# Performance work log

Hardware: AMD Instinct MI355X
Metric: run time of the kernel (lower is better)

Reference implementation:

```python
import jax, jax.numpy as jnp
import numpy as np

# Module config (matches init_kwargs)
IN_F = 4096
OUT_F = 12288
R = 16
ENABLE_LORA = [True, False, True]
N_BLOCKS = len(ENABLE_LORA)          # 3 fused output blocks (Q, K, V)
GROUPS = sum(ENABLE_LORA)            # 2 LoRA-enabled blocks
OUT_PG = OUT_F // N_BLOCKS           # 4096 rows per block
ENABLED_IDX = np.array([i for i, e in enumerate(ENABLE_LORA) if e])  # [0, 2]


def setup_inputs() -> dict:
    key = jax.random.key(0)
    kx, ka, kb = jax.random.split(key, 3)
    x = jax.random.normal(kx, (2, 512, IN_F), dtype=jnp.float32)
    # kaiming_uniform-like scale is irrelevant for correctness testing; use randn
    weight_A = jax.random.normal(ka, (GROUPS * R, IN_F), dtype=jnp.float32) * 0.02
    weight_B = jax.random.normal(kb, (OUT_PG * GROUPS, R), dtype=jnp.float32) * 0.02
    return {"x": x, "weight_A": weight_A, "weight_B": weight_B}


def _merge_AB(weight_A, weight_B):
    # grouped conv1d with kernel size 1 == per-group matmul B_g @ A_g
    A = weight_A.reshape(GROUPS, R, IN_F)          # (g, r, in)
    B = weight_B.reshape(GROUPS, OUT_PG, R)        # (g, out_pg, r)
    delta = jnp.einsum('gor,gri->goi', B, A)       # (g, out_pg, in)
    # zero_pad: scatter enabled blocks into the full (N_BLOCKS, out_pg, in) weight
    W = jnp.zeros((N_BLOCKS, OUT_PG, IN_F), dtype=delta.dtype)
    W = W.at[jnp.asarray(ENABLED_IDX)].set(delta)
    return W.reshape(OUT_F, IN_F)


def reference(x, weight_A, weight_B):
    W = _merge_AB(weight_A, weight_B)              # (out_f, in_f), full materialization as in torch
    return jnp.einsum('bsi,oi->bso', x, W)         # F.linear(x, W), no bias (lora_bias=False)
```

## Files before the change

kernel.cpp:

```cpp
#include <hip/hip_runtime.h>
#include <hip/hip_bf16.h>

#define IN_F   4096
#define OUT_F  12288
#define OUT_PG 4096
#define M_ROWS 1024
#define R2     32
#define KS     16

__global__ __launch_bounds__(256) void lora_a_kernel(
    const float* __restrict__ x, const float* __restrict__ wA,
    float* __restrict__ Tpart, float* __restrict__ out) {
  constexpr int SLICE = IN_F / KS;
  constexpr int ZC    = OUT_PG / KS;
  __shared__ float As[R2 * SLICE];

  const int t = threadIdx.x;
  const int l = t & 63;
  const int w = t >> 6;
  const int ks = blockIdx.x;
  const int row0 = blockIdx.y * 16 + w * 4;
  const int kb = ks * SLICE;

  {
    const int zrow0 = blockIdx.y * 16;
    const int zcol0 = OUT_PG + ks * ZC;
    const float4 z = {0.f, 0.f, 0.f, 0.f};
#pragma unroll
    for (int i = 0; i < 4; ++i) {
      const int idx = t + i * 256;
      const int zr = idx >> 6;
      const int zc = (idx & 63) * 4;
      *reinterpret_cast<float4*>(&out[(zrow0 + zr) * OUT_F + zcol0 + zc]) = z;
    }
  }

#pragma unroll
  for (int i = 0; i < 8; ++i) {
    const int f = t * 4 + i * 1024;
    const int r = f >> 8, kk = f & 255;
    *reinterpret_cast<float4*>(&As[f]) =
        *reinterpret_cast<const float4*>(&wA[r * IN_F + kb + kk]);
  }
  __syncthreads();

  float4 xv[4];
#pragma unroll
  for (int m = 0; m < 4; ++m)
    xv[m] = *reinterpret_cast<const float4*>(&x[(row0 + m) * IN_F + kb + l * 4]);

  float acc[4][32];
#pragma unroll
  for (int m = 0; m < 4; ++m)
#pragma unroll
    for (int r = 0; r < 32; ++r) acc[m][r] = 0.f;

#pragma unroll
  for (int r = 0; r < 32; ++r) {
    const float4 av = *reinterpret_cast<const float4*>(&As[r * SLICE + l * 4]);
#pragma unroll
    for (int m = 0; m < 4; ++m)
      acc[m][r] += xv[m].x * av.x + xv[m].y * av.y + xv[m].z * av.z + xv[m].w * av.w;
  }

  float v[4];
#pragma unroll
  for (int m2 = 0; m2 < 4; ++m2) {
#pragma unroll
    for (int m = 16; m >= 1; m >>= 1) {
#pragma unroll
      for (int i = 0; i < m; ++i) {
        const float a = acc[m2][i], b = acc[m2][i + m];
        const float mine   = (l & m) ? b : a;
        const float theirs = (l & m) ? a : b;
        acc[m2][i] = mine + __shfl_xor(theirs, m, 64);
      }
    }
    v[m2] = acc[m2][0] + __shfl_xor(acc[m2][0], 32, 64);
  }
#pragma unroll
  for (int p = 0; p < 2; ++p) {
    const float outv = (l < 32) ? v[2 * p] : v[2 * p + 1];
    Tpart[(ks * M_ROWS + row0 + 2 * p + (l >> 5)) * R2 + (l & 31)] = outv;
  }
}

__global__ __launch_bounds__(256) void lora_b_kernel(
    const float* __restrict__ Tpart, const float* __restrict__ wB,
    float* __restrict__ out) {
  const int t = threadIdx.x;
  const int bx = blockIdx.x;
  const int by = blockIdx.y;
  const int g = bx >> 4;
  const int jbase = (bx & 15) << 8;
  const int colbase = g ? (2 * OUT_PG + jbase) : jbase;
  const int rbase = by << 5;
  const int cq = t & 63;
  const int rowg = t >> 6;

  __shared__ float BsT[16 * 260];
  __shared__ float Ts[32 * 16];

#pragma unroll
  for (int i = 0; i < 4; ++i) {
    const int idx = t + i * 256;
    const int c = idx >> 2, r0 = (idx & 3) * 4;
    const float4 v = *reinterpret_cast<const float4*>(
        &wB[(g * OUT_PG + jbase + c) * 16 + r0]);
    BsT[(r0 + 0) * 260 + c] = v.x;
    BsT[(r0 + 1) * 260 + c] = v.y;
    BsT[(r0 + 2) * 260 + c] = v.z;
    BsT[(r0 + 3) * 260 + c] = v.w;
  }
  if (t < 128) {
    const int row = t >> 2, q = t & 3;
    float4 s0 = {0.f, 0.f, 0.f, 0.f}, s1 = {0.f, 0.f, 0.f, 0.f};
#pragma unroll
    for (int ks = 0; ks < KS; ks += 2) {
      const float4 v0 = *reinterpret_cast<const float4*>(
          &Tpart[((ks + 0) * M_ROWS + rbase + row) * R2 + g * 16 + q * 4]);
      const float4 v1 = *reinterpret_cast<const float4*>(
          &Tpart[((ks + 1) * M_ROWS + rbase + row) * R2 + g * 16 + q * 4]);
      s0.x += v0.x; s0.y += v0.y; s0.z += v0.z; s0.w += v0.w;
      s1.x += v1.x; s1.y += v1.y; s1.z += v1.z; s1.w += v1.w;
    }
    const float4 s = {s0.x + s1.x, s0.y + s1.y, s0.z + s1.z, s0.w + s1.w};
    *reinterpret_cast<float4*>(&Ts[row * 16 + q * 4]) = s;
  }
  __syncthreads();

  float4 brow[16];
#pragma unroll
  for (int r = 0; r < 16; ++r)
    brow[r] = *reinterpret_cast<const float4*>(&BsT[r * 260 + cq * 4]);

#pragma unroll
  for (int rr = 0; rr < 8; ++rr) {
    const int rowl = rowg * 8 + rr;
    float ts[16];
#pragma unroll
    for (int q = 0; q < 4; ++q)
      *reinterpret_cast<float4*>(&ts[q * 4]) =
          *reinterpret_cast<const float4*>(&Ts[rowl * 16 + q * 4]);
    float a0 = 0.f, a1 = 0.f, a2 = 0.f, a3 = 0.f;
#pragma unroll
    for (int r = 0; r < 16; ++r) {
      a0 += ts[r] * brow[r].x;
      a1 += ts[r] * brow[r].y;
      a2 += ts[r] * brow[r].z;
      a3 += ts[r] * brow[r].w;
    }
    const float4 accv = {a0, a1, a2, a3};
    *reinterpret_cast<float4*>(&out[(rbase + rowl) * OUT_F + colbase + cq * 4]) = accv;
  }
}

extern "C" void kernel_launch(void* const* d_in, const int* in_sizes, int n_in,
                              void* d_out, int out_size, void* d_ws, size_t ws_size,
                              hipStream_t stream) {
  const float* x  = (const float*)d_in[0];
  const float* wA = (const float*)d_in[1];
  const float* wB = (const float*)d_in[2];
  float* out = (float*)d_out;
  float* Tpart = (float*)d_ws;

  lora_a_kernel<<<dim3(KS, M_ROWS / 16), 256, 0, stream>>>(x, wA, Tpart, out);
  lora_b_kernel<<<dim3(32, M_ROWS / 32), 256, 0, stream>>>(Tpart, wB, out);
}
```

Before: 100.9 us.

## Add separate split-K reduction kernel and move zero-fill of the disabled block into it

Adds a third kernel that reduces the 16 split-K partial sums of T once per row and writes the final T to workspace. It also zeroes the disabled K output block, which the A kernel used to do. The B kernel now reads the reduced T directly instead of redoing the 16-way reduction in each of its 32 column blocks. The cost is an extra kernel launch and a serial dependency, in exchange for less redundant Tpart traffic and a lighter A kernel.

```diff
diff --git a/kernel.cpp b/kernel.cpp
--- a/kernel.cpp
+++ b/kernel.cpp
@@ -10,9 +10,8 @@
 
 __global__ __launch_bounds__(256) void lora_a_kernel(
     const float* __restrict__ x, const float* __restrict__ wA,
-    float* __restrict__ Tpart, float* __restrict__ out) {
+    float* __restrict__ Tpart) {
   constexpr int SLICE = IN_F / KS;
-  constexpr int ZC    = OUT_PG / KS;
   __shared__ float As[R2 * SLICE];
 
   const int t = threadIdx.x;
@@ -21,19 +20,6 @@
   const int ks = blockIdx.x;
   const int row0 = blockIdx.y * 16 + w * 4;
   const int kb = ks * SLICE;
-
-  {
-    const int zrow0 = blockIdx.y * 16;
-    const int zcol0 = OUT_PG + ks * ZC;
-    const float4 z = {0.f, 0.f, 0.f, 0.f};
-#pragma unroll
-    for (int i = 0; i < 4; ++i) {
-      const int idx = t + i * 256;
-      const int zr = idx >> 6;
-      const int zc = (idx & 63) * 4;
-      *reinterpret_cast<float4*>(&out[(zrow0 + zr) * OUT_F + zcol0 + zc]) = z;
-    }
-  }
 
 #pragma unroll
   for (int i = 0; i < 8; ++i) {
@@ -85,8 +71,45 @@
   }
 }
 
+__global__ __launch_bounds__(256) void lora_r_kernel(
+    const float* __restrict__ Tpart, float* __restrict__ T,
+    float* __restrict__ out) {
+  const int t = threadIdx.x;
+  const int row0 = blockIdx.x * 4;
+
+  {
+    const float4 z = {0.f, 0.f, 0.f, 0.f};
+    const int zr = row0 + (t >> 6);
+    const int c0 = OUT_PG + (t & 63) * 4;
+#pragma unroll
+    for (int i = 0; i < 16; ++i)
+      *reinterpret_cast<float4*>(&out[zr * OUT_F + c0 + i * 256]) = z;
+  }
+
+  __shared__ float4 red[32][8];
+  const int e   = t >> 3;
+  const int ksl = t & 7;
+  const int row = row0 + (e >> 3);
+  const int q   = (e & 7) * 4;
+  const float4 v0 = *reinterpret_cast<const float4*>(
+      &Tpart[((ksl + 0) * M_ROWS + row) * R2 + q]);
+  const float4 v1 = *reinterpret_cast<const float4*>(
+      &Tpart[((ksl + 8) * M_ROWS + row) * R2 + q]);
+  red[e][ksl] = {v0.x + v1.x, v0.y + v1.y, v0.z + v1.z, v0.w + v1.w};
+  __syncthreads();
+  if (t < 32) {
+    float4 s = red[t][0];
+#pragma unroll
+    for (int i = 1; i < 8; ++i) {
+      const float4 v = red[t][i];
+      s.x += v.x; s.y += v.y; s.z += v.z; s.w += v.w;
+    }
+    *reinterpret_cast<float4*>(&T[(row0 + (t >> 3)) * R2 + (t & 7) * 4]) = s;
+  }
+}
+
 __global__ __launch_bounds__(256) void lora_b_kernel(
-    const float* __restrict__ Tpart, const float* __restrict__ wB,
+    const float* __restrict__ T, const float* __restrict__ wB,
     float* __restrict__ out) {
   const int t = threadIdx.x;
   const int bx = blockIdx.x;
@@ -114,18 +137,8 @@
   }
   if (t < 128) {
     const int row = t >> 2, q = t & 3;
-    float4 s0 = {0.f, 0.f, 0.f, 0.f}, s1 = {0.f, 0.f, 0.f, 0.f};
-#pragma unroll
-    for (int ks = 0; ks < KS; ks += 2) {
-      const float4 v0 = *reinterpret_cast<const float4*>(
-          &Tpart[((ks + 0) * M_ROWS + rbase + row) * R2 + g * 16 + q * 4]);
-      const float4 v1 = *reinterpret_cast<const float4*>(
-          &Tpart[((ks + 1) * M_ROWS + rbase + row) * R2 + g * 16 + q * 4]);
-      s0.x += v0.x; s0.y += v0.y; s0.z += v0.z; s0.w += v0.w;
-      s1.x += v1.x; s1.y += v1.y; s1.z += v1.z; s1.w += v1.w;
-    }
-    const float4 s = {s0.x + s1.x, s0.y + s1.y, s0.z + s1.z, s0.w + s1.w};
-    *reinterpret_cast<float4*>(&Ts[row * 16 + q * 4]) = s;
+    *reinterpret_cast<float4*>(&Ts[row * 16 + q * 4]) =
+        *reinterpret_cast<const float4*>(&T[(rbase + row) * R2 + g * 16 + q * 4]);
   }
   __syncthreads();
 
@@ -163,7 +176,9 @@
   const float* wB = (const float*)d_in[2];
   float* out = (float*)d_out;
   float* Tpart = (float*)d_ws;
+  float* T = Tpart + (size_t)KS * M_ROWS * R2;
 
-  lora_a_kernel<<<dim3(KS, M_ROWS / 16), 256, 0, stream>>>(x, wA, Tpart, out);
-  lora_b_kernel<<<dim3(32, M_ROWS / 32), 256, 0, stream>>>(Tpart, wB, out);
+  lora_a_kernel<<<dim3(KS, M_ROWS / 16), 256, 0, stream>>>(x, wA, Tpart);
+  lora_r_kernel<<<dim3(M_ROWS / 4), 256, 0, stream>>>(Tpart, T, out);
+  lora_b_kernel<<<dim3(32, M_ROWS / 32), 256, 0, stream>>>(T, wB, out);
 }
```

Measured after the change: 102.1 us. No clear change (+1.2%).

## Fuse LoRA A and B stages into one persistent kernel with grid barrier

Applied to the files above, without the earlier changes.

The two kernels are merged into a single persistent kernel of 512 blocks. Each block processes two A-stage tiles, then waits at a global atomic-counter barrier before processing two B-stage tiles. The goal is to remove the second kernel launch and the gap between kernels. In exchange it adds a memset launch for the counter and a spin barrier. The barrier deadlocks unless all 512 blocks are co-resident, which the launch_bounds(256,2) hint is meant to help ensure.

```diff
diff --git a/kernel.cpp b/kernel.cpp
--- a/kernel.cpp
+++ b/kernel.cpp
@@ -7,151 +7,171 @@
 #define M_ROWS 1024
 #define R2     32
 #define KS     16
+#define NBLK   512
 
-__global__ __launch_bounds__(256) void lora_a_kernel(
+__global__ __launch_bounds__(256, 2) void lora_fused_kernel(
     const float* __restrict__ x, const float* __restrict__ wA,
-    float* __restrict__ Tpart, float* __restrict__ out) {
-  constexpr int SLICE = IN_F / KS;
-  constexpr int ZC    = OUT_PG / KS;
-  __shared__ float As[R2 * SLICE];
+    const float* __restrict__ wB, float* __restrict__ Tpart,
+    float* __restrict__ out, unsigned* __restrict__ counter) {
+  __shared__ float shmem[R2 * 256];
 
   const int t = threadIdx.x;
   const int l = t & 63;
   const int w = t >> 6;
-  const int ks = blockIdx.x;
-  const int row0 = blockIdx.y * 16 + w * 4;
-  const int kb = ks * SLICE;
 
-  {
-    const int zrow0 = blockIdx.y * 16;
-    const int zcol0 = OUT_PG + ks * ZC;
-    const float4 z = {0.f, 0.f, 0.f, 0.f};
+  float* As = shmem;
+#pragma unroll 1
+  for (int i2 = 0; i2 < 2; ++i2) {
+    const int tau = (int)blockIdx.x + i2 * NBLK;
+    const int ks = tau >> 6;
+    const int rg = tau & 63;
+    const int row0 = rg * 16 + w * 4;
+    const int kb = ks * 256;
+
+    {
+      const int zrow0 = rg * 16;
+      const int zcol0 = OUT_PG + ks * 256;
+      const float4 z = {0.f, 0.f, 0.f, 0.f};
+#pragma unroll
+      for (int i = 0; i < 4; ++i) {
+        const int idx = t + i * 256;
+        const int zr = idx >> 6;
+        const int zc = (idx & 63) * 4;
+        *reinterpret_cast<float4*>(&out[(zrow0 + zr) * OUT_F + zcol0 + zc]) = z;
+      }
+    }
+
+    float4 xv[4];
+#pragma unroll
+    for (int m = 0; m < 4; ++m)
+      xv[m] = *reinterpret_cast<const float4*>(&x[(row0 + m) * IN_F + kb + l * 4]);
+
+    if (i2) __syncthreads();
+#pragma unroll
+    for (int i = 0; i < 8; ++i) {
+      const int f = t * 4 + i * 1024;
+      const int r = f >> 8, kk = f & 255;
+      *reinterpret_cast<float4*>(&As[f]) =
+          *reinterpret_cast<const float4*>(&wA[r * IN_F + kb + kk]);
+    }
+    __syncthreads();
+
+    float acc[4][32];
+#pragma unroll
+    for (int m = 0; m < 4; ++m)
+#pragma unroll
+      for (int r = 0; r < 32; ++r) acc[m][r] = 0.f;
+
+#pragma unroll
+    for (int r = 0; r < 32; ++r) {
+      const float4 av = *reinterpret_cast<const float4*>(&As[r * 256 + l * 4]);
+#pragma unroll
+      for (int m = 0; m < 4; ++m)
+        acc[m][r] += xv[m].x * av.x + xv[m].y * av.y + xv[m].z * av.z + xv[m].w * av.w;
+    }
+
+    float v[4];
+#pragma unroll
+    for (int m2 = 0; m2 < 4; ++m2) {
+#pragma unroll
+      for (int m = 16; m >= 1; m >>= 1) {
+#pragma unroll
+        for (int i = 0; i < m; ++i) {
+          const float a = acc[m2][i], b = acc[m2][i + m];
+          const float mine   = (l & m) ? b : a;
+          const float theirs = (l & m) ? a : b;
+          acc[m2][i] = mine + __shfl_xor(theirs, m, 64);
+        }
+      }
+      v[m2] = acc[m2][0] + __shfl_xor(acc[m2][0], 32, 64);
+    }
+#pragma unroll
+    for (int p = 0; p < 2; ++p) {
+      const float outv = (l < 32) ? v[2 * p] : v[2 * p + 1];
+      Tpart[(ks * M_ROWS + row0 + 2 * p + (l >> 5)) * R2 + (l & 31)] = outv;
+    }
+  }
+
+  __syncthreads();
+  if (t == 0) {
+    __hip_atomic_fetch_add(counter, 1u, __ATOMIC_RELEASE, __HIP_MEMORY_SCOPE_AGENT);
+    while (__hip_atomic_load(counter, __ATOMIC_ACQUIRE, __HIP_MEMORY_SCOPE_AGENT)
+           < (unsigned)NBLK) {
+      __builtin_amdgcn_s_sleep(8);
+    }
+  }
+  __syncthreads();
+
+  float* BsT = shmem;
+  float* Ts  = shmem + 16 * 260;
+  const int cq = t & 63;
+  const int rowg = t >> 6;
+
+#pragma unroll 1
+  for (int i2 = 0; i2 < 2; ++i2) {
+    const int u = (int)blockIdx.x + i2 * NBLK;
+    const int bxc = u >> 5;
+    const int by  = u & 31;
+    const int g = bxc >> 4;
+    const int jbase = (bxc & 15) << 8;
+    const int colbase = g ? (2 * OUT_PG + jbase) : jbase;
+    const int rbase = by << 5;
+
+    if (i2) __syncthreads();
 #pragma unroll
     for (int i = 0; i < 4; ++i) {
       const int idx = t + i * 256;
-      const int zr = idx >> 6;
-      const int zc = (idx & 63) * 4;
-      *reinterpret_cast<float4*>(&out[(zrow0 + zr) * OUT_F + zcol0 + zc]) = z;
+      const int c = idx >> 2, r0 = (idx & 3) * 4;
+      const float4 vv = *reinterpret_cast<const float4*>(
+          &wB[(g * OUT_PG + jbase + c) * 16 + r0]);
+      BsT[(r0 + 0) * 260 + c] = vv.x;
+      BsT[(r0 + 1) * 260 + c] = vv.y;
+      BsT[(r0 + 2) * 260 + c] = vv.z;
+      BsT[(r0 + 3) * 260 + c] = vv.w;
     }
-  }
+    if (t < 128) {
+      const int row = t >> 2, q = t & 3;
+      float4 s0 = {0.f, 0.f, 0.f, 0.f}, s1 = {0.f, 0.f, 0.f, 0.f};
+#pragma unroll
+      for (int ks = 0; ks < KS; ks += 2) {
+        const float4 v0 = *reinterpret_cast<const float4*>(
+            &Tpart[((ks + 0) * M_ROWS + rbase + row) * R2 + g * 16 + q * 4]);
+        const float4 v1 = *reinterpret_cast<const float4*>(
+            &Tpart[((ks + 1) * M_ROWS + rbase + row) * R2 + g * 16 + q * 4]);
+        s0.x += v0.x; s0.y += v0.y; s0.z += v0.z; s0.w += v0.w;
+        s1.x += v1.x; s1.y += v1.y; s1.z += v1.z; s1.w += v1.w;
+      }
+      Ts[row * 16 + q * 4 + 0] = s0.x + s1.x;
+      Ts[row * 16 + q * 4 + 1] = s0.y + s1.y;
+      Ts[row * 16 + q * 4 + 2] = s0.z + s1.z;
+      Ts[row * 16 + q * 4 + 3] = s0.w + s1.w;
+    }
+    __syncthreads();
+
+    float4 brow[16];
+#pragma unroll
+    for (int r = 0; r < 16; ++r)
+      brow[r] = *reinterpret_cast<const float4*>(&BsT[r * 260 + cq * 4]);
 
 #pragma unroll
-  for (int i = 0; i < 8; ++i) {
-    const int f = t * 4 + i * 1024;
-    const int r = f >> 8, kk = f & 255;
-    *reinterpret_cast<float4*>(&As[f]) =
-        *reinterpret_cast<const float4*>(&wA[r * IN_F + kb + kk]);
-  }
-  __syncthreads();
-
-  float4 xv[4];
+    for (int rr = 0; rr < 8; ++rr) {
+      const int rowl = rowg * 8 + rr;
+      float ts[16];
 #pragma unroll
-  for (int m = 0; m < 4; ++m)
-    xv[m] = *reinterpret_cast<const float4*>(&x[(row0 + m) * IN_F + kb + l * 4]);
-
-  float acc[4][32];
+      for (int q = 0; q < 4; ++q)
+        *reinterpret_cast<float4*>(&ts[q * 4]) =
+            *reinterpret_cast<const float4*>(&Ts[rowl * 16 + q * 4]);
+      float a0 = 0.f, a1 = 0.f, a2 = 0.f, a3 = 0.f;
 #pragma unroll
-  for (int m = 0; m < 4; ++m)
-#pragma unroll
-    for (int r = 0; r < 32; ++r) acc[m][r] = 0.f;
-
-#pragma unroll
-  for (int r = 0; r < 32; ++r) {
-    const float4 av = *reinterpret_cast<const float4*>(&As[r * SLICE + l * 4]);
-#pragma unroll
-    for (int m = 0; m < 4; ++m)
-      acc[m][r] += xv[m].x * av.x + xv[m].y * av.y + xv[m].z * av.z + xv[m].w * av.w;
-  }
-
-  float v[4];
-#pragma unroll
-  for (int m2 = 0; m2 < 4; ++m2) {
-#pragma unroll
-    for (int m = 16; m >= 1; m >>= 1) {
-#pragma unroll
-      for (int i = 0; i < m; ++i) {
-        const float a = acc[m2][i], b = acc[m2][i + m];
-        const float mine   = (l & m) ? b : a;
-        const float theirs = (l & m) ? a : b;
-        acc[m2][i] = mine + __shfl_xor(theirs, m, 64);
+      for (int r = 0; r < 16; ++r) {
+        a0 += ts[r] * brow[r].x;
+        a1 += ts[r] * brow[r].y;
+        a2 += ts[r] * brow[r].z;
+        a3 += ts[r] * brow[r].w;
       }
+      const float4 accv = {a0, a1, a2, a3};
+      *reinterpret_cast<float4*>(&out[(rbase + rowl) * OUT_F + colbase + cq * 4]) = accv;
     }
-    v[m2] = acc[m2][0] + __shfl_xor(acc[m2][0], 32, 64);
-  }
-#pragma unroll
-  for (int p = 0; p < 2; ++p) {
-    const float outv = (l < 32) ? v[2 * p] : v[2 * p + 1];
-    Tpart[(ks * M_ROWS + row0 + 2 * p + (l >> 5)) * R2 + (l & 31)] = outv;
-  }
-}
-
-__global__ __launch_bounds__(256) void lora_b_kernel(
-    const float* __restrict__ Tpart, const float* __restrict__ wB,
-    float* __restrict__ out) {
-  const int t = threadIdx.x;
-  const int bx = blockIdx.x;
-  const int by = blockIdx.y;
-  const int g = bx >> 4;
-  const int jbase = (bx & 15) << 8;
-  const int colbase = g ? (2 * OUT_PG + jbase) : jbase;
-  const int rbase = by << 5;
-  const int cq = t & 63;
-  const int rowg = t >> 6;
-
-  __shared__ float BsT[16 * 260];
-  __shared__ float Ts[32 * 16];
-
-#pragma unroll
-  for (int i = 0; i < 4; ++i) {
-    const int idx = t + i * 256;
-    const int c = idx >> 2, r0 = (idx & 3) * 4;
-    const float4 v = *reinterpret_cast<const float4*>(
-        &wB[(g * OUT_PG + jbase + c) * 16 + r0]);
-    BsT[(r0 + 0) * 260 + c] = v.x;
-    BsT[(r0 + 1) * 260 + c] = v.y;
-    BsT[(r0 + 2) * 260 + c] = v.z;
-    BsT[(r0 + 3) * 260 + c] = v.w;
-  }
-  if (t < 128) {
-    const int row = t >> 2, q = t & 3;
-    float4 s0 = {0.f, 0.f, 0.f, 0.f}, s1 = {0.f, 0.f, 0.f, 0.f};
-#pragma unroll
-    for (int ks = 0; ks < KS; ks += 2) {
-      const float4 v0 = *reinterpret_cast<const float4*>(
-          &Tpart[((ks + 0) * M_ROWS + rbase + row) * R2 + g * 16 + q * 4]);
-      const float4 v1 = *reinterpret_cast<const float4*>(
-          &Tpart[((ks + 1) * M_ROWS + rbase + row) * R2 + g * 16 + q * 4]);
-      s0.x += v0.x; s0.y += v0.y; s0.z += v0.z; s0.w += v0.w;
-      s1.x += v1.x; s1.y += v1.y; s1.z += v1.z; s1.w += v1.w;
-    }
-    const float4 s = {s0.x + s1.x, s0.y + s1.y, s0.z + s1.z, s0.w + s1.w};
-    *reinterpret_cast<float4*>(&Ts[row * 16 + q * 4]) = s;
-  }
-  __syncthreads();
-
-  float4 brow[16];
-#pragma unroll
-  for (int r = 0; r < 16; ++r)
-    brow[r] = *reinterpret_cast<const float4*>(&BsT[r * 260 + cq * 4]);
-
-#pragma unroll
-  for (int rr = 0; rr < 8; ++rr) {
-    const int rowl = rowg * 8 + rr;
-    float ts[16];
-#pragma unroll
-    for (int q = 0; q < 4; ++q)
-      *reinterpret_cast<float4*>(&ts[q * 4]) =
-          *reinterpret_cast<const float4*>(&Ts[rowl * 16 + q * 4]);
-    float a0 = 0.f, a1 = 0.f, a2 = 0.f, a3 = 0.f;
-#pragma unroll
-    for (int r = 0; r < 16; ++r) {
-      a0 += ts[r] * brow[r].x;
-      a1 += ts[r] * brow[r].y;
-      a2 += ts[r] * brow[r].z;
-      a3 += ts[r] * brow[r].w;
-    }
-    const float4 accv = {a0, a1, a2, a3};
-    *reinterpret_cast<float4*>(&out[(rbase + rowl) * OUT_F + colbase + cq * 4]) = accv;
   }
 }
 
@@ -163,7 +183,8 @@
   const float* wB = (const float*)d_in[2];
   float* out = (float*)d_out;
   float* Tpart = (float*)d_ws;
+  unsigned* counter = (unsigned*)(Tpart + (size_t)KS * M_ROWS * R2);
 
-  lora_a_kernel<<<dim3(KS, M_ROWS / 16), 256, 0, stream>>>(x, wA, Tpart, out);
-  lora_b_kernel<<<dim3(32, M_ROWS / 32), 256, 0, stream>>>(Tpart, wB, out);
+  hipMemsetAsync(counter, 0, 64, stream);
+  lora_fused_kernel<<<NBLK, 256, 0, stream>>>(x, wA, wB, Tpart, out, counter);
 }
```

New measurement: 137.1 us. 35.9% more time.
